# Performance work log

Measured on AMD Instinct MI355X. Metric: run time of the kernel, lower is better.

## Reference

```python
import jax, jax.numpy as jnp
import numpy as np


def bilinear_sampler(img, flow):
    """Warp img (B,H,W,C) by per-pixel flow (B,H,W,2): sample at (x+u, y+v).
    Border handling: indices clipped to the image (edge padding)."""
    B, H, W, C = img.shape
    gy, gx = jnp.meshgrid(jnp.arange(H, dtype=img.dtype),
                          jnp.arange(W, dtype=img.dtype), indexing='ij')
    x = gx[None] + flow[..., 0]  # (B,H,W)
    y = gy[None] + flow[..., 1]
    x0f = jnp.floor(x)
    y0f = jnp.floor(y)
    wx = x - x0f  # fractional parts, differentiable w.r.t. flow
    wy = y - y0f
    x0 = jnp.clip(x0f.astype(jnp.int32), 0, W - 1)
    x1 = jnp.clip(x0f.astype(jnp.int32) + 1, 0, W - 1)
    y0 = jnp.clip(y0f.astype(jnp.int32), 0, H - 1)
    y1 = jnp.clip(y0f.astype(jnp.int32) + 1, 0, H - 1)
    b = jnp.arange(B)[:, None, None]
    Ia = img[b, y0, x0]  # (B,H,W,C)
    Ib = img[b, y1, x0]
    Ic = img[b, y0, x1]
    Id = img[b, y1, x1]
    wx = wx[..., None]
    wy = wy[..., None]
    return (Ia * (1 - wx) * (1 - wy) + Ib * (1 - wx) * wy
            + Ic * wx * (1 - wy) + Id * wx * wy)


def setup_inputs() -> dict:
    key = jax.random.key(0)
    k1, k2, k3, k4, k5, k6 = jax.random.split(key, 6)
    B, H, W = 8, 512, 512
    return {
        't': jax.random.uniform(k1, (B, 1, 1, 1), dtype=jnp.float32),
        'I0': jax.random.uniform(k2, (B, H, W, 3), dtype=jnp.float32),
        'I1': jax.random.uniform(k3, (B, H, W, 3), dtype=jnp.float32),
        'interp': jax.random.normal(k4, (B, H, W, 5), dtype=jnp.float32),
        'Fhat_t0': jax.random.normal(k5, (B, H, W, 2), dtype=jnp.float32),
        'Fhat_t1': jax.random.normal(k6, (B, H, W, 2), dtype=jnp.float32),
    }


def reference(t, I0, I1, interp, Fhat_t0, Fhat_t1):
    Ft0 = interp[..., 0:2] + Fhat_t0
    Ft1 = interp[..., 2:4] + Fhat_t1
    Vt0 = jax.nn.sigmoid(interp[..., 4:5])  # (B,H,W,1) -> broadcasts over RGB
    Vt1 = 1.0 - Vt0
    g0 = bilinear_sampler(I0, Ft0)
    g1 = bilinear_sampler(I1, Ft1)
    eps = 1e-12
    w0 = (1.0 - t) * Vt0
    w1 = t * Vt1
    It = (w0 * g0 + w1 * g1) / (w0 + w1 + eps)
    return It
```

## Files before the change

kernel.cpp:

```cpp
#include <hip/hip_runtime.h>
#include <hip/hip_fp16.h>

constexpr int B_ = 8;
constexpr int H_ = 512;
constexpr int W_ = 512;
constexpr int HW_ = H_ * W_;

constexpr int TS = 32;
constexpr int R_ = 6;
constexpr int RS = TS + 2 * R_;
constexpr int NSPX = RS * RS;


template <int IMG>
__device__ __forceinline__ void sampleT(const __half2* __restrict__ rgp,
                                        const __half2* __restrict__ bbp,
                                        const float* __restrict__ img,
                                        int gx0, int gy0,
                                        float sx, float sy, float g[3]) {
    float xf = floorf(sx), yf = floorf(sy);
    float wx = sx - xf, wy = sy - yf;
    int ix = (int)xf, iy = (int)yf;
    int x0 = min(max(ix, 0), W_ - 1);
    int x1 = min(max(ix + 1, 0), W_ - 1);
    int y0 = min(max(iy, 0), H_ - 1);
    int y1 = min(max(iy + 1, 0), H_ - 1);

    float w00 = (1.0f - wx) * (1.0f - wy);
    float w01 = wx * (1.0f - wy);
    float w10 = (1.0f - wx) * wy;
    float w11 = wx * wy;

    int lx0 = x0 - gx0, lx1 = x1 - gx0;
    int ly0 = y0 - gy0, ly1 = y1 - gy0;
    bool inT = ((unsigned)lx0 < (unsigned)RS) & ((unsigned)lx1 < (unsigned)RS) &
               ((unsigned)ly0 < (unsigned)RS) & ((unsigned)ly1 < (unsigned)RS);

    if (inT) {
        int p00 = ly0 * RS + lx0, p01 = ly0 * RS + lx1;
        int p10 = ly1 * RS + lx0, p11 = ly1 * RS + lx1;
        __half2 h00 = __float2half2_rn(w00);
        __half2 h01 = __float2half2_rn(w01);
        __half2 h10 = __float2half2_rn(w10);
        __half2 h11 = __float2half2_rn(w11);
        __half2 rg = __hmul2(h00, rgp[p00]);
        rg = __hfma2(h01, rgp[p01], rg);
        rg = __hfma2(h10, rgp[p10], rg);
        rg = __hfma2(h11, rgp[p11], rg);
        __half2 bb = __hmul2(h00, bbp[p00]);
        bb = __hfma2(h01, bbp[p01], bb);
        bb = __hfma2(h10, bbp[p10], bb);
        bb = __hfma2(h11, bbp[p11], bb);
        g[0] = __low2float(rg);
        g[1] = __high2float(rg);
        g[2] = (IMG == 0) ? __low2float(bb) : __high2float(bb);
    } else {
        const float* pa = img + ((size_t)y0 * W_ + x0) * 3;
        const float* pb = img + ((size_t)y0 * W_ + x1) * 3;
        const float* pc = img + ((size_t)y1 * W_ + x0) * 3;
        const float* pd = img + ((size_t)y1 * W_ + x1) * 3;
        #pragma unroll
        for (int ch = 0; ch < 3; ++ch)
            g[ch] = pa[ch] * w00 + pb[ch] * w01 +
                    pc[ch] * w10 + pd[ch] * w11;
    }
}

__global__ __launch_bounds__(256, 6) void frame_interp_tiled(
    const float* __restrict__ t,
    const float* __restrict__ I0,
    const float* __restrict__ I1,
    const float* __restrict__ interp,
    const float* __restrict__ F0,
    const float* __restrict__ F1,
    float* __restrict__ out)
{
    __shared__ __half2 lds_rg[2][NSPX];
    __shared__ __half2 lds_bb[NSPX];

    int tid = threadIdx.x;
    int bid = blockIdx.x;
    int b    = bid & 7;
    int tile = bid >> 3;
    int ty   = tile >> 4;
    int tx   = tile & 15;
    int gx0 = tx * TS - R_;
    int gy0 = ty * TS - R_;

    const float* img0 = I0 + (size_t)b * HW_ * 3;
    const float* img1 = I1 + (size_t)b * HW_ * 3;

    float tb = t[b];

    #pragma unroll
    for (int k = 0; k < (NSPX + 255) / 256; ++k) {
        int p = tid + k * 256;
        if (p < NSPX) {
            int ry = p / RS;
            int rx = p - ry * RS;
            int gy = min(max(gy0 + ry, 0), H_ - 1);
            int gx = min(max(gx0 + rx, 0), W_ - 1);
            size_t s = ((size_t)gy * W_ + gx) * 3;
            float c0[3], c1[3];
            __builtin_memcpy(c0, img0 + s, 12);
            __builtin_memcpy(c1, img1 + s, 12);
            lds_rg[0][p] = __floats2half2_rn(c0[0], c0[1]);
            lds_rg[1][p] = __floats2half2_rn(c1[0], c1[1]);
            lds_bb[p]    = __floats2half2_rn(c0[2], c1[2]);
        }
    }
    __syncthreads();

    #pragma unroll
    for (int k = 0; k < 4; ++k) {
        int p   = tid + k * 256;
        int row = p >> 5;
        int col = p & 31;
        int gx = tx * TS + col;
        int gy = ty * TS + row;
        int idx = b * HW_ + gy * W_ + gx;

        const float* ip = interp + (size_t)idx * 5;
        float i01[2], i23[2];
        __builtin_memcpy(i01, ip, 8);
        __builtin_memcpy(i23, ip + 2, 8);
        float i4 = ip[4];
        float2 f0 = *(const float2*)(F0 + (size_t)idx * 2);
        float2 f1 = *(const float2*)(F1 + (size_t)idx * 2);

        float ft0x = i01[0] + f0.x;
        float ft0y = i01[1] + f0.y;
        float ft1x = i23[0] + f1.x;
        float ft1y = i23[1] + f1.y;
        float vt0  = 1.0f / (1.0f + __expf(-i4));

        float g0[3], g1[3];
        sampleT<0>(lds_rg[0], lds_bb, img0, gx0, gy0,
                   (float)gx + ft0x, (float)gy + ft0y, g0);
        sampleT<1>(lds_rg[1], lds_bb, img1, gx0, gy0,
                   (float)gx + ft1x, (float)gy + ft1y, g1);

        float w0 = (1.0f - tb) * vt0;
        float w1 = tb * (1.0f - vt0);
        float inv = 1.0f / (w0 + w1 + 1e-12f);

        float o[3];
        o[0] = (w0 * g0[0] + w1 * g1[0]) * inv;
        o[1] = (w0 * g0[1] + w1 * g1[1]) * inv;
        o[2] = (w0 * g0[2] + w1 * g1[2]) * inv;
        __builtin_memcpy(out + (size_t)idx * 3, o, 12);
    }
}

extern "C" void kernel_launch(void* const* d_in, const int* in_sizes, int n_in,
                              void* d_out, int out_size, void* d_ws, size_t ws_size,
                              hipStream_t stream) {
    const float* t      = (const float*)d_in[0];
    const float* I0     = (const float*)d_in[1];
    const float* I1     = (const float*)d_in[2];
    const float* interp = (const float*)d_in[3];
    const float* F0     = (const float*)d_in[4];
    const float* F1     = (const float*)d_in[5];
    float* out = (float*)d_out;

    int blocks = B_ * (H_ / TS) * (W_ / TS);
    frame_interp_tiled<<<blocks, 256, 0, stream>>>(t, I0, I1, interp, F0, F1, out);
}
```

Before: 163.9 us.

## Replace LDS-tiled fp16 sampling with direct global gathers and vectorized per-thread pixels

Removes the shared-memory halo tile (and its fp16 conversion and barrier), so bilinear taps are read straight from global memory and served by the caches. Each thread now handles four consecutive pixels in a row, so interp, flow and output accesses become wide contiguous vector loads and stores. Blocks are ordered to interleave batches. This drops the LDS staging cost and the fp16 precision loss, but every tap now goes to L1/L2 instead of LDS, and occupancy hints are lowered.

```diff
diff --git a/kernel.cpp b/kernel.cpp
--- a/kernel.cpp
+++ b/kernel.cpp
@@ -1,22 +1,12 @@
 #include <hip/hip_runtime.h>
-#include <hip/hip_fp16.h>
 
 constexpr int B_ = 8;
 constexpr int H_ = 512;
 constexpr int W_ = 512;
 constexpr int HW_ = H_ * W_;
 
-constexpr int TS = 32;
-constexpr int R_ = 6;
-constexpr int RS = TS + 2 * R_;
-constexpr int NSPX = RS * RS;
 
-
-template <int IMG>
-__device__ __forceinline__ void sampleT(const __half2* __restrict__ rgp,
-                                        const __half2* __restrict__ bbp,
-                                        const float* __restrict__ img,
-                                        int gx0, int gy0,
+__device__ __forceinline__ void sampleG(const float* __restrict__ img,
                                         float sx, float sy, float g[3]) {
     float xf = floorf(sx), yf = floorf(sy);
     float wx = sx - xf, wy = sy - yf;
@@ -31,42 +21,17 @@
     float w10 = (1.0f - wx) * wy;
     float w11 = wx * wy;
 
-    int lx0 = x0 - gx0, lx1 = x1 - gx0;
-    int ly0 = y0 - gy0, ly1 = y1 - gy0;
-    bool inT = ((unsigned)lx0 < (unsigned)RS) & ((unsigned)lx1 < (unsigned)RS) &
-               ((unsigned)ly0 < (unsigned)RS) & ((unsigned)ly1 < (unsigned)RS);
-
-    if (inT) {
-        int p00 = ly0 * RS + lx0, p01 = ly0 * RS + lx1;
-        int p10 = ly1 * RS + lx0, p11 = ly1 * RS + lx1;
-        __half2 h00 = __float2half2_rn(w00);
-        __half2 h01 = __float2half2_rn(w01);
-        __half2 h10 = __float2half2_rn(w10);
-        __half2 h11 = __float2half2_rn(w11);
-        __half2 rg = __hmul2(h00, rgp[p00]);
-        rg = __hfma2(h01, rgp[p01], rg);
-        rg = __hfma2(h10, rgp[p10], rg);
-        rg = __hfma2(h11, rgp[p11], rg);
-        __half2 bb = __hmul2(h00, bbp[p00]);
-        bb = __hfma2(h01, bbp[p01], bb);
-        bb = __hfma2(h10, bbp[p10], bb);
-        bb = __hfma2(h11, bbp[p11], bb);
-        g[0] = __low2float(rg);
-        g[1] = __high2float(rg);
-        g[2] = (IMG == 0) ? __low2float(bb) : __high2float(bb);
-    } else {
-        const float* pa = img + ((size_t)y0 * W_ + x0) * 3;
-        const float* pb = img + ((size_t)y0 * W_ + x1) * 3;
-        const float* pc = img + ((size_t)y1 * W_ + x0) * 3;
-        const float* pd = img + ((size_t)y1 * W_ + x1) * 3;
-        #pragma unroll
-        for (int ch = 0; ch < 3; ++ch)
-            g[ch] = pa[ch] * w00 + pb[ch] * w01 +
-                    pc[ch] * w10 + pd[ch] * w11;
-    }
+    float a[3], bv[3], c[3], d[3];
+    __builtin_memcpy(a,  img + ((size_t)y0 * W_ + x0) * 3, 12);
+    __builtin_memcpy(bv, img + ((size_t)y0 * W_ + x1) * 3, 12);
+    __builtin_memcpy(c,  img + ((size_t)y1 * W_ + x0) * 3, 12);
+    __builtin_memcpy(d,  img + ((size_t)y1 * W_ + x1) * 3, 12);
+    #pragma unroll
+    for (int ch = 0; ch < 3; ++ch)
+        g[ch] = a[ch] * w00 + bv[ch] * w01 + c[ch] * w10 + d[ch] * w11;
 }
 
-__global__ __launch_bounds__(256, 6) void frame_interp_tiled(
+__global__ __launch_bounds__(256, 4) void frame_interp_gather(
     const float* __restrict__ t,
     const float* __restrict__ I0,
     const float* __restrict__ I1,
@@ -75,81 +40,47 @@
     const float* __restrict__ F1,
     float* __restrict__ out)
 {
-    __shared__ __half2 lds_rg[2][NSPX];
-    __shared__ __half2 lds_bb[NSPX];
-
-    int tid = threadIdx.x;
     int bid = blockIdx.x;
-    int b    = bid & 7;
-    int tile = bid >> 3;
-    int ty   = tile >> 4;
-    int tx   = tile & 15;
-    int gx0 = tx * TS - R_;
-    int gy0 = ty * TS - R_;
+    int nb = (bid & 7) * 256 + (bid >> 3);
+    size_t q0 = (size_t)nb * 1024 + (size_t)threadIdx.x * 4;
+    int b   = (int)(q0 >> 18);
+    int pix = (int)(q0 & (size_t)(HW_ - 1));
+    int gy  = pix >> 9;
+    int gxb = pix & 511;
 
     const float* img0 = I0 + (size_t)b * HW_ * 3;
     const float* img1 = I1 + (size_t)b * HW_ * 3;
-
     float tb = t[b];
 
-    #pragma unroll
-    for (int k = 0; k < (NSPX + 255) / 256; ++k) {
-        int p = tid + k * 256;
-        if (p < NSPX) {
-            int ry = p / RS;
-            int rx = p - ry * RS;
-            int gy = min(max(gy0 + ry, 0), H_ - 1);
-            int gx = min(max(gx0 + rx, 0), W_ - 1);
-            size_t s = ((size_t)gy * W_ + gx) * 3;
-            float c0[3], c1[3];
-            __builtin_memcpy(c0, img0 + s, 12);
-            __builtin_memcpy(c1, img1 + s, 12);
-            lds_rg[0][p] = __floats2half2_rn(c0[0], c0[1]);
-            lds_rg[1][p] = __floats2half2_rn(c1[0], c1[1]);
-            lds_bb[p]    = __floats2half2_rn(c0[2], c1[2]);
-        }
-    }
-    __syncthreads();
+    float ii[20];
+    __builtin_memcpy(ii, interp + q0 * 5, 80);
+    float f0v[8], f1v[8];
+    __builtin_memcpy(f0v, F0 + q0 * 2, 32);
+    __builtin_memcpy(f1v, F1 + q0 * 2, 32);
 
+    float o[12];
     #pragma unroll
     for (int k = 0; k < 4; ++k) {
-        int p   = tid + k * 256;
-        int row = p >> 5;
-        int col = p & 31;
-        int gx = tx * TS + col;
-        int gy = ty * TS + row;
-        int idx = b * HW_ + gy * W_ + gx;
-
-        const float* ip = interp + (size_t)idx * 5;
-        float i01[2], i23[2];
-        __builtin_memcpy(i01, ip, 8);
-        __builtin_memcpy(i23, ip + 2, 8);
-        float i4 = ip[4];
-        float2 f0 = *(const float2*)(F0 + (size_t)idx * 2);
-        float2 f1 = *(const float2*)(F1 + (size_t)idx * 2);
-
-        float ft0x = i01[0] + f0.x;
-        float ft0y = i01[1] + f0.y;
-        float ft1x = i23[0] + f1.x;
-        float ft1y = i23[1] + f1.y;
-        float vt0  = 1.0f / (1.0f + __expf(-i4));
+        float fx = (float)(gxb + k);
+        float fy = (float)gy;
+        float sx0 = fx + ii[k * 5 + 0] + f0v[k * 2 + 0];
+        float sy0 = fy + ii[k * 5 + 1] + f0v[k * 2 + 1];
+        float sx1 = fx + ii[k * 5 + 2] + f1v[k * 2 + 0];
+        float sy1 = fy + ii[k * 5 + 3] + f1v[k * 2 + 1];
+        float vt0 = 1.0f / (1.0f + __expf(-ii[k * 5 + 4]));
 
         float g0[3], g1[3];
-        sampleT<0>(lds_rg[0], lds_bb, img0, gx0, gy0,
-                   (float)gx + ft0x, (float)gy + ft0y, g0);
-        sampleT<1>(lds_rg[1], lds_bb, img1, gx0, gy0,
-                   (float)gx + ft1x, (float)gy + ft1y, g1);
+        sampleG(img0, sx0, sy0, g0);
+        sampleG(img1, sx1, sy1, g1);
 
         float w0 = (1.0f - tb) * vt0;
         float w1 = tb * (1.0f - vt0);
         float inv = 1.0f / (w0 + w1 + 1e-12f);
-
-        float o[3];
-        o[0] = (w0 * g0[0] + w1 * g1[0]) * inv;
-        o[1] = (w0 * g0[1] + w1 * g1[1]) * inv;
-        o[2] = (w0 * g0[2] + w1 * g1[2]) * inv;
-        __builtin_memcpy(out + (size_t)idx * 3, o, 12);
+        o[k * 3 + 0] = (w0 * g0[0] + w1 * g1[0]) * inv;
+        o[k * 3 + 1] = (w0 * g0[1] + w1 * g1[1]) * inv;
+        o[k * 3 + 2] = (w0 * g0[2] + w1 * g1[2]) * inv;
     }
+    __builtin_memcpy(out + q0 * 3, o, 48);
 }
 
 extern "C" void kernel_launch(void* const* d_in, const int* in_sizes, int n_in,
@@ -163,6 +94,6 @@
     const float* F1     = (const float*)d_in[5];
     float* out = (float*)d_out;
 
-    int blocks = B_ * (H_ / TS) * (W_ / TS);
-    frame_interp_tiled<<<blocks, 256, 0, stream>>>(t, I0, I1, interp, F0, F1, out);
+    int blocks = (B_ * HW_) / (256 * 4);
+    frame_interp_gather<<<blocks, 256, 0, stream>>>(t, I0, I1, interp, F0, F1, out);
 }
```

Result: slower. 223.7 us (+36.5%).
